# Kernel tuning notes

Measured on AMD Instinct MI355X. Metric: run time of the kernel, lower is better.

## Reference

```python
import jax, jax.numpy as jnp
import numpy as np

NUM_HEADS = 8
NG = 8  # group/grid size: seq = NG**3 = 512


def setup_inputs() -> dict:
    key = jax.random.key(0)
    k1, k2, k3 = jax.random.split(key, 3)
    batch, seq, chan = 32, NG ** 3, 512
    subspace_dim = 24
    x = jax.random.normal(k1, (batch, seq, chan), jnp.float32)
    # fixed symmetric-subspace basis (the free variable `conv_kernel` in the source)
    basis = jax.random.normal(k2, (seq, subspace_dim), jnp.float32)
    # learned param: (subspace_dim, num_heads), init stddev 0.01
    kernel = jax.random.normal(k3, (subspace_dim, NUM_HEADS), jnp.float32) * 0.01
    return {"x": x, "basis": basis, "kernel": kernel}


def reference(x, basis, kernel):
    batch, seq, chan = x.shape
    h, ng = NUM_HEADS, NG
    kn = 2 * ng - 1  # 15: circular tiling window
    ch = chan // h
    # 'batch (8 8 8) (ch h) -> h (batch ch) 8 8 8'
    x_im = x.reshape(batch, ng, ng, ng, ch, h)
    x_im = jnp.transpose(x_im, (5, 0, 4, 1, 2, 3)).reshape(h, batch * ch, ng, ng, ng)
    # circular tiling: tile 2x2x2 then crop to 2*ng-1 per axis; add trailing C=1
    x_im = jnp.tile(x_im, (1, 1, 2, 2, 2))[:, :, :kn, :kn, :kn, None]
    # expand subspace kernel: '(n n n) s, s h -> h n n n 1 1'
    kexp = jnp.einsum('gs,sh->hg', basis, kernel).reshape(h, ng, ng, ng, 1, 1)

    def conv(lhs, rhs):
        return jax.lax.conv_general_dilated(
            lhs, rhs, window_strides=(1, 1, 1), padding='VALID',
            dimension_numbers=('NXYZC', 'XYZIO', 'NXYZC'))

    # per-head VALID conv: [batch*ch, 15,15,15, 1] * [8,8,8,1,1] -> [batch*ch, 8,8,8, 1]
    out = jax.vmap(conv)(x_im, kexp)[..., 0]  # [h, batch*ch, 8, 8, 8]
    # 'h (batch ch) n n n -> batch (n n n) (ch h)'
    out = out.reshape(h, batch, ch, seq)
    out = jnp.transpose(out, (1, 3, 2, 0)).reshape(batch, seq, chan)
    return out
```

## Files before the change

### kernel.cpp

```cpp
#include <hip/hip_runtime.h>


#define S2C 0.70710678118654752f
#define SIGSTRIDE 577

template <bool INV>
__device__ __forceinline__ void dft8(float* R, float* I)
{
    float t0r = R[0] + R[4], t0i = I[0] + I[4];
    float t1r = R[1] + R[5], t1i = I[1] + I[5];
    float t2r = R[2] + R[6], t2i = I[2] + I[6];
    float t3r = R[3] + R[7], t3i = I[3] + I[7];
    float b0r = R[0] - R[4], b0i = I[0] - I[4];
    float d1r = R[1] - R[5], d1i = I[1] - I[5];
    float d2r = R[2] - R[6], d2i = I[2] - I[6];
    float d3r = R[3] - R[7], d3i = I[3] - I[7];
    float b1r, b1i, b2r, b2i, b3r, b3i;
    if (!INV) {
        b1r = (d1r + d1i) * S2C;  b1i = (d1i - d1r) * S2C;
        b2r = d2i;                b2i = -d2r;
        b3r = (d3i - d3r) * S2C;  b3i = -(d3r + d3i) * S2C;
    } else {
        b1r = (d1r - d1i) * S2C;  b1i = (d1i + d1r) * S2C;
        b2r = -d2i;               b2i = d2r;
        b3r = -(d3r + d3i) * S2C; b3i = (d3r - d3i) * S2C;
    }
    float u0r = t0r + t2r, u0i = t0i + t2i;
    float u1r = t1r + t3r, u1i = t1i + t3i;
    float u2r = t0r - t2r, u2i = t0i - t2i;
    float e3r = t1r - t3r, e3i = t1i - t3i;
    float u3r, u3i;
    if (!INV) { u3r = e3i;  u3i = -e3r; }
    else      { u3r = -e3i; u3i = e3r;  }
    R[0] = u0r + u1r; I[0] = u0i + u1i;
    R[4] = u0r - u1r; I[4] = u0i - u1i;
    R[2] = u2r + u3r; I[2] = u2i + u3i;
    R[6] = u2r - u3r; I[6] = u2i - u3i;
    float v0r = b0r + b2r, v0i = b0i + b2i;
    float v1r = b1r + b3r, v1i = b1i + b3i;
    float v2r = b0r - b2r, v2i = b0i - b2i;
    float w3r = b1r - b3r, w3i = b1i - b3i;
    float v3r, v3i;
    if (!INV) { v3r = w3i;  v3i = -w3r; }
    else      { v3r = -w3i; v3i = w3r;  }
    R[1] = v0r + v1r; I[1] = v0i + v1i;
    R[5] = v0r - v1r; I[5] = v0i - v1i;
    R[3] = v2r + v3r; I[3] = v2i + v3i;
    R[7] = v2r - v3r; I[7] = v2i - v3i;
}

__device__ const float CTAB8[8] = {1.f, S2C, 0.f, -S2C, -1.f, -S2C, 0.f, S2C};
__device__ const float STAB8[8] = {0.f, S2C, 1.f, S2C, 0.f, -S2C, -1.f, -S2C};

__global__ __launch_bounds__(256)
void eqfft_prep(const float* __restrict__ basis,
                const float* __restrict__ kparam,
                float2* __restrict__ V)
{
    __shared__ float Wl[512];
    __shared__ float CT[8], ST[8];
    const int tid = threadIdx.x;
    const int blk = blockIdx.x;
    const int h   = blk >> 4;
    if (tid < 8) { CT[tid] = CTAB8[tid]; ST[tid] = STAB8[tid]; }
    #pragma unroll
    for (int t = 0; t < 2; ++t) {
        const int g = tid * 2 + t;
        const float* bp = basis + g * 24;
        float acc = 0.f;
        #pragma unroll
        for (int s = 0; s < 24; ++s) acc += bp[s] * kparam[s * 8 + h];
        Wl[(g & 63) * 8 + (g >> 6)] = acc;
    }
    __syncthreads();
    const int f  = (blk & 15) * 32 + (tid >> 3);
    const int g1 = tid & 7;
    const int f1 = f >> 6, f2 = (f >> 3) & 7, f3 = f & 7;
    const int kb = (f1 * g1) & 7;
    float pr = 0.f, pi = 0.f;
    for (int g2 = 0; g2 < 8; ++g2) {
        const int k2 = kb + f2 * g2;
        const float* wrow = &Wl[g2 * 64 + g1];
        #pragma unroll
        for (int g3 = 0; g3 < 8; ++g3) {
            const int k = (k2 + f3 * g3) & 7;
            const float w = wrow[g3 * 8];
            pr += w * CT[k];
            pi += w * ST[k];
        }
    }
    pr += __shfl_xor(pr, 1); pi += __shfl_xor(pi, 1);
    pr += __shfl_xor(pr, 2); pi += __shfl_xor(pi, 2);
    pr += __shfl_xor(pr, 4); pi += __shfl_xor(pi, 4);
    if (g1 == 0)
        V[h * 512 + f] = make_float2(pr * (1.f / 512.f), pi * (1.f / 512.f));
}

__global__ __launch_bounds__(512, 6)
void eqfft_main(const float* __restrict__ x,
                const float2* __restrict__ V,
                float* __restrict__ out)
{
    __shared__ float reA[8 * SIGSTRIDE];
    __shared__ float imA[8 * SIGSTRIDE];

    const int tid  = threadIdx.x;
    const int bid  = blockIdx.x;
    const int L    = (bid & 7) * 256 + (bid >> 3);
    const int b    = L >> 6;
    const int ch0  = (L & 63) * 8;
    const int wid  = tid >> 6;
    const int lane = tid & 63;

    const float* xb = x  + (size_t)b * 262144 + ch0;
    float*       ob = out + (size_t)b * 262144 + ch0;

    #pragma unroll
    for (int i = 0; i < 2; ++i) {
        const int v  = i * 512 + tid;
        const int p  = v >> 1;
        const int c4 = (v & 1) * 4;
        const float4 d = *(const float4*)(xb + p * 512 + c4);
        const int base = (p >> 6) * 72 + ((p >> 3) & 7) * 9 + (p & 7);
        reA[(c4 + 0) * SIGSTRIDE + base] = d.x;
        reA[(c4 + 1) * SIGSTRIDE + base] = d.y;
        reA[(c4 + 2) * SIGSTRIDE + base] = d.z;
        reA[(c4 + 3) * SIGSTRIDE + base] = d.w;
    }
    __syncthreads();

    {
        const int base = wid * SIGSTRIDE + (lane >> 3) * 72 + (lane & 7) * 9;
        float R[8], I[8];
        #pragma unroll
        for (int j = 0; j < 8; ++j) { R[j] = reA[base + j]; I[j] = 0.f; }
        dft8<false>(R, I);
        #pragma unroll
        for (int j = 0; j < 8; ++j) { reA[base + j] = R[j]; imA[base + j] = I[j]; }
    }
    __syncthreads();

    {
        const int base = wid * SIGSTRIDE + (lane >> 3) * 72 + (lane & 7);
        float R[8], I[8];
        #pragma unroll
        for (int j = 0; j < 8; ++j) { R[j] = reA[base + j * 9]; I[j] = imA[base + j * 9]; }
        dft8<false>(R, I);
        #pragma unroll
        for (int j = 0; j < 8; ++j) { reA[base + j * 9] = R[j]; imA[base + j * 9] = I[j]; }
    }
    __syncthreads();

    {
        const int p2 = lane >> 3, p3 = lane & 7;
        const int base = wid * SIGSTRIDE + p2 * 9 + p3;
        const float2* vp = V + (wid << 9) + (p2 << 3) + p3;
        float R[8], I[8];
        #pragma unroll
        for (int j = 0; j < 8; ++j) { R[j] = reA[base + j * 72]; I[j] = imA[base + j * 72]; }
        dft8<false>(R, I);
        #pragma unroll
        for (int j = 0; j < 8; ++j) {
            const float2 v = vp[j << 6];
            const float nr = R[j] * v.x - I[j] * v.y;
            I[j] = R[j] * v.y + I[j] * v.x;
            R[j] = nr;
        }
        dft8<true>(R, I);
        #pragma unroll
        for (int j = 0; j < 8; ++j) { reA[base + j * 72] = R[j]; imA[base + j * 72] = I[j]; }
    }
    __syncthreads();

    {
        const int base = wid * SIGSTRIDE + (lane >> 3) * 72 + (lane & 7);
        float R[8], I[8];
        #pragma unroll
        for (int j = 0; j < 8; ++j) { R[j] = reA[base + j * 9]; I[j] = imA[base + j * 9]; }
        dft8<true>(R, I);
        #pragma unroll
        for (int j = 0; j < 8; ++j) { reA[base + j * 9] = R[j]; imA[base + j * 9] = I[j]; }
    }
    __syncthreads();

    {
        const int base = wid * SIGSTRIDE + (lane >> 3) * 72 + (lane & 7) * 9;
        float R[8], I[8];
        #pragma unroll
        for (int j = 0; j < 8; ++j) { R[j] = reA[base + j]; I[j] = imA[base + j]; }
        dft8<true>(R, I);
        #pragma unroll
        for (int j = 0; j < 8; ++j) { reA[base + j] = R[j]; }
    }
    __syncthreads();

    #pragma unroll
    for (int i = 0; i < 2; ++i) {
        const int v  = i * 512 + tid;
        const int p  = v >> 1;
        const int c4 = (v & 1) * 4;
        const int base = (p >> 6) * 72 + ((p >> 3) & 7) * 9 + (p & 7);
        float4 d;
        d.x = reA[(c4 + 0) * SIGSTRIDE + base];
        d.y = reA[(c4 + 1) * SIGSTRIDE + base];
        d.z = reA[(c4 + 2) * SIGSTRIDE + base];
        d.w = reA[(c4 + 3) * SIGSTRIDE + base];
        *(float4*)(ob + p * 512 + c4) = d;
    }
}

extern "C" void kernel_launch(void* const* d_in, const int* in_sizes, int n_in,
                              void* d_out, int out_size, void* d_ws, size_t ws_size,
                              hipStream_t stream)
{
    const float* x      = (const float*)d_in[0];
    const float* basis  = (const float*)d_in[1];
    const float* kparam = (const float*)d_in[2];
    float* out          = (float*)d_out;
    float2* V           = (float2*)d_ws;

    hipLaunchKernelGGL(eqfft_prep, dim3(128),  dim3(256), 0, stream, basis, kparam, V);
    hipLaunchKernelGGL(eqfft_main, dim3(2048), dim3(512), 0, stream, x, V, out);
}
```

Measured before the change: 98.13 us.

## Pack channel pairs interleaved in LDS and process two FFTs per thread

Reorganizes the shared-memory signal layout so each pair of channels is interleaved (float2), letting each thread run two 3D-FFT lines at once with vectorized float2/float4 LDS accesses. Block size drops from 512 to 256 threads with 3 blocks per CU, and the block-index swizzle is removed. This aims to cut LDS instruction count and bank traffic, and to raise per-thread ILP. The cost is more registers per thread and a different occupancy/L2 access pattern.

```diff
diff --git a/kernel.cpp b/kernel.cpp
--- a/kernel.cpp
+++ b/kernel.cpp
@@ -2,7 +2,9 @@
 
 
 #define S2C 0.70710678118654752f
-#define SIGSTRIDE 577
+#define ST2 20
+#define ST1 164
+#define STP 1312
 
 template <bool INV>
 __device__ __forceinline__ void dft8(float* R, float* I)
@@ -96,116 +98,155 @@
         V[h * 512 + f] = make_float2(pr * (1.f / 512.f), pi * (1.f / 512.f));
 }
 
-__global__ __launch_bounds__(512, 6)
+__global__ __launch_bounds__(256, 3)
 void eqfft_main(const float* __restrict__ x,
                 const float2* __restrict__ V,
                 float* __restrict__ out)
 {
-    __shared__ float reA[8 * SIGSTRIDE];
-    __shared__ float imA[8 * SIGSTRIDE];
-
-    const int tid  = threadIdx.x;
-    const int bid  = blockIdx.x;
-    const int L    = (bid & 7) * 256 + (bid >> 3);
-    const int b    = L >> 6;
-    const int ch0  = (L & 63) * 8;
-    const int wid  = tid >> 6;
-    const int lane = tid & 63;
-
-    const float* xb = x  + (size_t)b * 262144 + ch0;
+    __shared__ __align__(16) float reA[4 * STP];
+    __shared__ __align__(16) float imA[4 * STP];
+
+    const int tid = threadIdx.x;
+    const int bid = blockIdx.x;
+    const int b   = bid >> 6;
+    const int ch0 = (bid & 63) * 8;
+
+    const float* xb = x   + (size_t)b * 262144 + ch0;
     float*       ob = out + (size_t)b * 262144 + ch0;
 
     #pragma unroll
-    for (int i = 0; i < 2; ++i) {
-        const int v  = i * 512 + tid;
-        const int p  = v >> 1;
+    for (int i = 0; i < 4; ++i) {
+        const int v  = i * 256 + tid;
+        const int pt = v >> 1;
         const int c4 = (v & 1) * 4;
-        const float4 d = *(const float4*)(xb + p * 512 + c4);
-        const int base = (p >> 6) * 72 + ((p >> 3) & 7) * 9 + (p & 7);
-        reA[(c4 + 0) * SIGSTRIDE + base] = d.x;
-        reA[(c4 + 1) * SIGSTRIDE + base] = d.y;
-        reA[(c4 + 2) * SIGSTRIDE + base] = d.z;
-        reA[(c4 + 3) * SIGSTRIDE + base] = d.w;
-    }
-    __syncthreads();
-
-    {
-        const int base = wid * SIGSTRIDE + (lane >> 3) * 72 + (lane & 7) * 9;
-        float R[8], I[8];
-        #pragma unroll
-        for (int j = 0; j < 8; ++j) { R[j] = reA[base + j]; I[j] = 0.f; }
-        dft8<false>(R, I);
-        #pragma unroll
-        for (int j = 0; j < 8; ++j) { reA[base + j] = R[j]; imA[base + j] = I[j]; }
-    }
-    __syncthreads();
-
-    {
-        const int base = wid * SIGSTRIDE + (lane >> 3) * 72 + (lane & 7);
-        float R[8], I[8];
-        #pragma unroll
-        for (int j = 0; j < 8; ++j) { R[j] = reA[base + j * 9]; I[j] = imA[base + j * 9]; }
-        dft8<false>(R, I);
-        #pragma unroll
-        for (int j = 0; j < 8; ++j) { reA[base + j * 9] = R[j]; imA[base + j * 9] = I[j]; }
-    }
-    __syncthreads();
-
-    {
-        const int p2 = lane >> 3, p3 = lane & 7;
-        const int base = wid * SIGSTRIDE + p2 * 9 + p3;
-        const float2* vp = V + (wid << 9) + (p2 << 3) + p3;
-        float R[8], I[8];
-        #pragma unroll
-        for (int j = 0; j < 8; ++j) { R[j] = reA[base + j * 72]; I[j] = imA[base + j * 72]; }
-        dft8<false>(R, I);
-        #pragma unroll
-        for (int j = 0; j < 8; ++j) {
-            const float2 v = vp[j << 6];
-            const float nr = R[j] * v.x - I[j] * v.y;
-            I[j] = R[j] * v.y + I[j] * v.x;
-            R[j] = nr;
-        }
-        dft8<true>(R, I);
-        #pragma unroll
-        for (int j = 0; j < 8; ++j) { reA[base + j * 72] = R[j]; imA[base + j * 72] = I[j]; }
-    }
-    __syncthreads();
-
-    {
-        const int base = wid * SIGSTRIDE + (lane >> 3) * 72 + (lane & 7);
-        float R[8], I[8];
-        #pragma unroll
-        for (int j = 0; j < 8; ++j) { R[j] = reA[base + j * 9]; I[j] = imA[base + j * 9]; }
-        dft8<true>(R, I);
-        #pragma unroll
-        for (int j = 0; j < 8; ++j) { reA[base + j * 9] = R[j]; imA[base + j * 9] = I[j]; }
-    }
-    __syncthreads();
-
-    {
-        const int base = wid * SIGSTRIDE + (lane >> 3) * 72 + (lane & 7) * 9;
-        float R[8], I[8];
-        #pragma unroll
-        for (int j = 0; j < 8; ++j) { R[j] = reA[base + j]; I[j] = imA[base + j]; }
-        dft8<true>(R, I);
-        #pragma unroll
-        for (int j = 0; j < 8; ++j) { reA[base + j] = R[j]; }
+        const float4 d = *(const float4*)(xb + pt * 512 + c4);
+        const int base = (pt >> 6) * ST1 + ((pt >> 3) & 7) * ST2 + (pt & 7) * 2;
+        const int pr = c4 >> 1;
+        *(float2*)(reA + pr * STP + base)       = make_float2(d.x, d.y);
+        *(float2*)(reA + (pr + 1) * STP + base) = make_float2(d.z, d.w);
+    }
+    __syncthreads();
+
+    const int pair = tid >> 6;
+    const int line = tid & 63;
+    float R0[8], I0[8], R1[8], I1[8];
+
+    {
+        float* rp = reA + pair * STP + (line >> 3) * ST1 + (line & 7) * ST2;
+        float* ip = imA + pair * STP + (line >> 3) * ST1 + (line & 7) * ST2;
+        #pragma unroll
+        for (int k = 0; k < 4; ++k) {
+            const float4 d = *(const float4*)(rp + 4 * k);
+            R0[2*k] = d.x; R1[2*k] = d.y; R0[2*k+1] = d.z; R1[2*k+1] = d.w;
+            I0[2*k] = 0.f; I1[2*k] = 0.f; I0[2*k+1] = 0.f; I1[2*k+1] = 0.f;
+        }
+        dft8<false>(R0, I0); dft8<false>(R1, I1);
+        #pragma unroll
+        for (int k = 0; k < 4; ++k) {
+            *(float4*)(rp + 4*k) = make_float4(R0[2*k], R1[2*k], R0[2*k+1], R1[2*k+1]);
+            *(float4*)(ip + 4*k) = make_float4(I0[2*k], I1[2*k], I0[2*k+1], I1[2*k+1]);
+        }
+    }
+    __syncthreads();
+
+    {
+        float* rp = reA + pair * STP + (line >> 3) * ST1 + (line & 7) * 2;
+        float* ip = imA + pair * STP + (line >> 3) * ST1 + (line & 7) * 2;
+        #pragma unroll
+        for (int j = 0; j < 8; ++j) {
+            const float2 a = *(const float2*)(rp + j * ST2);
+            const float2 c = *(const float2*)(ip + j * ST2);
+            R0[j] = a.x; R1[j] = a.y; I0[j] = c.x; I1[j] = c.y;
+        }
+        dft8<false>(R0, I0); dft8<false>(R1, I1);
+        #pragma unroll
+        for (int j = 0; j < 8; ++j) {
+            *(float2*)(rp + j * ST2) = make_float2(R0[j], R1[j]);
+            *(float2*)(ip + j * ST2) = make_float2(I0[j], I1[j]);
+        }
+    }
+    __syncthreads();
+
+    {
+        const int p2 = line >> 3, p3 = line & 7;
+        const float2* v0 = V + (pair * 2 + 0) * 512 + p2 * 8 + p3;
+        const float2* v1 = V + (pair * 2 + 1) * 512 + p2 * 8 + p3;
+        float2 va[8], vb[8];
+        #pragma unroll
+        for (int j = 0; j < 8; ++j) { va[j] = v0[j << 6]; vb[j] = v1[j << 6]; }
+
+        float* rp = reA + pair * STP + p2 * ST2 + p3 * 2;
+        float* ip = imA + pair * STP + p2 * ST2 + p3 * 2;
+        #pragma unroll
+        for (int j = 0; j < 8; ++j) {
+            const float2 a = *(const float2*)(rp + j * ST1);
+            const float2 c = *(const float2*)(ip + j * ST1);
+            R0[j] = a.x; R1[j] = a.y; I0[j] = c.x; I1[j] = c.y;
+        }
+        dft8<false>(R0, I0); dft8<false>(R1, I1);
+        #pragma unroll
+        for (int j = 0; j < 8; ++j) {
+            float nr = R0[j] * va[j].x - I0[j] * va[j].y;
+            I0[j]    = R0[j] * va[j].y + I0[j] * va[j].x;
+            R0[j]    = nr;
+            nr       = R1[j] * vb[j].x - I1[j] * vb[j].y;
+            I1[j]    = R1[j] * vb[j].y + I1[j] * vb[j].x;
+            R1[j]    = nr;
+        }
+        dft8<true>(R0, I0); dft8<true>(R1, I1);
+        #pragma unroll
+        for (int j = 0; j < 8; ++j) {
+            *(float2*)(rp + j * ST1) = make_float2(R0[j], R1[j]);
+            *(float2*)(ip + j * ST1) = make_float2(I0[j], I1[j]);
+        }
+    }
+    __syncthreads();
+
+    {
+        float* rp = reA + pair * STP + (line >> 3) * ST1 + (line & 7) * 2;
+        float* ip = imA + pair * STP + (line >> 3) * ST1 + (line & 7) * 2;
+        #pragma unroll
+        for (int j = 0; j < 8; ++j) {
+            const float2 a = *(const float2*)(rp + j * ST2);
+            const float2 c = *(const float2*)(ip + j * ST2);
+            R0[j] = a.x; R1[j] = a.y; I0[j] = c.x; I1[j] = c.y;
+        }
+        dft8<true>(R0, I0); dft8<true>(R1, I1);
+        #pragma unroll
+        for (int j = 0; j < 8; ++j) {
+            *(float2*)(rp + j * ST2) = make_float2(R0[j], R1[j]);
+            *(float2*)(ip + j * ST2) = make_float2(I0[j], I1[j]);
+        }
+    }
+    __syncthreads();
+
+    {
+        float* rp = reA + pair * STP + (line >> 3) * ST1 + (line & 7) * ST2;
+        float* ip = imA + pair * STP + (line >> 3) * ST1 + (line & 7) * ST2;
+        #pragma unroll
+        for (int k = 0; k < 4; ++k) {
+            const float4 a = *(const float4*)(rp + 4 * k);
+            const float4 c = *(const float4*)(ip + 4 * k);
+            R0[2*k] = a.x; R1[2*k] = a.y; R0[2*k+1] = a.z; R1[2*k+1] = a.w;
+            I0[2*k] = c.x; I1[2*k] = c.y; I0[2*k+1] = c.z; I1[2*k+1] = c.w;
+        }
+        dft8<true>(R0, I0); dft8<true>(R1, I1);
+        #pragma unroll
+        for (int k = 0; k < 4; ++k)
+            *(float4*)(rp + 4*k) = make_float4(R0[2*k], R1[2*k], R0[2*k+1], R1[2*k+1]);
     }
     __syncthreads();
 
     #pragma unroll
-    for (int i = 0; i < 2; ++i) {
-        const int v  = i * 512 + tid;
-        const int p  = v >> 1;
+    for (int i = 0; i < 4; ++i) {
+        const int v  = i * 256 + tid;
+        const int pt = v >> 1;
         const int c4 = (v & 1) * 4;
-        const int base = (p >> 6) * 72 + ((p >> 3) & 7) * 9 + (p & 7);
-        float4 d;
-        d.x = reA[(c4 + 0) * SIGSTRIDE + base];
-        d.y = reA[(c4 + 1) * SIGSTRIDE + base];
-        d.z = reA[(c4 + 2) * SIGSTRIDE + base];
-        d.w = reA[(c4 + 3) * SIGSTRIDE + base];
-        *(float4*)(ob + p * 512 + c4) = d;
+        const int base = (pt >> 6) * ST1 + ((pt >> 3) & 7) * ST2 + (pt & 7) * 2;
+        const int pr = c4 >> 1;
+        const float2 a = *(const float2*)(reA + pr * STP + base);
+        const float2 c = *(const float2*)(reA + (pr + 1) * STP + base);
+        *(float4*)(ob + pt * 512 + c4) = make_float4(a.x, a.y, c.x, c.y);
     }
 }
 
@@ -220,5 +261,5 @@
     float2* V           = (float2*)d_ws;
 
     hipLaunchKernelGGL(eqfft_prep, dim3(128),  dim3(256), 0, stream, basis, kparam, V);
-    hipLaunchKernelGGL(eqfft_main, dim3(2048), dim3(512), 0, stream, x, V, out);
-}
+    hipLaunchKernelGGL(eqfft_main, dim3(2048), dim3(256), 0, stream, x, V, out);
+}
```

Result: slower. 113.8 us (+16.0%).

## Pack two real channels per complex FFT and interleave re/im in LDS

Applied to the files above, without the earlier changes.

Instead of running a complex 3D FFT on each real channel with zero imaginary part, the kernel packs two channels that share a head (c and c+8) into the real and imaginary parts of one complex signal. This halves the FFT work and the thread count per block. Re/im are interleaved in LDS so reads and writes can use float2/float4. Block-to-tile mapping and channel grouping are redone so each block handles four heads with paired channels. This relies on the filter being real so the two outputs can be separated from the real and imaginary parts, and the new LDS strides may change bank conflicts.

```diff
diff --git a/kernel.cpp b/kernel.cpp
--- a/kernel.cpp
+++ b/kernel.cpp
@@ -1,8 +1,10 @@
 #include <hip/hip_runtime.h>
 
 
-#define S2C 0.70710678118654752f
-#define SIGSTRIDE 577
+#define S2C  0.70710678118654752f
+#define LS2  16
+#define LS1  132
+#define LCST 1056
 
 template <bool INV>
 __device__ __forceinline__ void dft8(float* R, float* I)
@@ -96,116 +98,123 @@
         V[h * 512 + f] = make_float2(pr * (1.f / 512.f), pi * (1.f / 512.f));
 }
 
-__global__ __launch_bounds__(512, 6)
+__global__ __launch_bounds__(256, 6)
 void eqfft_main(const float* __restrict__ x,
                 const float2* __restrict__ V,
                 float* __restrict__ out)
 {
-    __shared__ float reA[8 * SIGSTRIDE];
-    __shared__ float imA[8 * SIGSTRIDE];
-
-    const int tid  = threadIdx.x;
-    const int bid  = blockIdx.x;
-    const int L    = (bid & 7) * 256 + (bid >> 3);
-    const int b    = L >> 6;
-    const int ch0  = (L & 63) * 8;
-    const int wid  = tid >> 6;
-    const int lane = tid & 63;
-
-    const float* xb = x  + (size_t)b * 262144 + ch0;
-    float*       ob = out + (size_t)b * 262144 + ch0;
+    __shared__ __align__(16) float lds[4 * LCST];
+
+    const int tid = threadIdx.x;
+    const int d   = blockIdx.x;
+    const int T   = (d & 7) * 2 + ((d >> 3) & 1) + (d >> 4) * 16;
+    const int b   = T >> 6;
+    const int r   = T & 63;
+    const int c0  = (r >> 1) * 16 + (r & 1) * 4;
+
+    const float* xb = x   + (size_t)b * 262144 + c0;
+    float*       ob = out + (size_t)b * 262144 + c0;
 
     #pragma unroll
     for (int i = 0; i < 2; ++i) {
-        const int v  = i * 512 + tid;
-        const int p  = v >> 1;
-        const int c4 = (v & 1) * 4;
-        const float4 d = *(const float4*)(xb + p * 512 + c4);
-        const int base = (p >> 6) * 72 + ((p >> 3) & 7) * 9 + (p & 7);
-        reA[(c4 + 0) * SIGSTRIDE + base] = d.x;
-        reA[(c4 + 1) * SIGSTRIDE + base] = d.y;
-        reA[(c4 + 2) * SIGSTRIDE + base] = d.z;
-        reA[(c4 + 3) * SIGSTRIDE + base] = d.w;
-    }
-    __syncthreads();
-
-    {
-        const int base = wid * SIGSTRIDE + (lane >> 3) * 72 + (lane & 7) * 9;
-        float R[8], I[8];
-        #pragma unroll
-        for (int j = 0; j < 8; ++j) { R[j] = reA[base + j]; I[j] = 0.f; }
+        const int p = i * 256 + tid;
+        const float4 A  = *(const float4*)(xb + p * 512);
+        const float4 Bv = *(const float4*)(xb + p * 512 + 8);
+        float* dst = lds + (p >> 6) * LS1 + ((p >> 3) & 7) * LS2 + (p & 7) * 2;
+        *(float2*)(dst + 0 * LCST) = make_float2(A.x, Bv.x);
+        *(float2*)(dst + 1 * LCST) = make_float2(A.y, Bv.y);
+        *(float2*)(dst + 2 * LCST) = make_float2(A.z, Bv.z);
+        *(float2*)(dst + 3 * LCST) = make_float2(A.w, Bv.w);
+    }
+    __syncthreads();
+
+    const int q    = tid >> 6;
+    const int lane = tid & 63;
+    const int hi   = lane >> 3, lo = lane & 7;
+    float* const cb = lds + q * LCST;
+    float R[8], I[8];
+
+    {
+        float* pp = cb + hi * LS1 + lo * LS2;
+        #pragma unroll
+        for (int k = 0; k < 4; ++k) {
+            const float4 z = *(const float4*)(pp + 4 * k);
+            R[2*k] = z.x; I[2*k] = z.y; R[2*k+1] = z.z; I[2*k+1] = z.w;
+        }
         dft8<false>(R, I);
         #pragma unroll
-        for (int j = 0; j < 8; ++j) { reA[base + j] = R[j]; imA[base + j] = I[j]; }
-    }
-    __syncthreads();
-
-    {
-        const int base = wid * SIGSTRIDE + (lane >> 3) * 72 + (lane & 7);
-        float R[8], I[8];
-        #pragma unroll
-        for (int j = 0; j < 8; ++j) { R[j] = reA[base + j * 9]; I[j] = imA[base + j * 9]; }
+        for (int k = 0; k < 4; ++k)
+            *(float4*)(pp + 4 * k) = make_float4(R[2*k], I[2*k], R[2*k+1], I[2*k+1]);
+    }
+    __syncthreads();
+
+    {
+        float* pp = cb + hi * LS1 + lo * 2;
+        #pragma unroll
+        for (int j = 0; j < 8; ++j) { const float2 z = *(const float2*)(pp + j * LS2); R[j] = z.x; I[j] = z.y; }
         dft8<false>(R, I);
         #pragma unroll
-        for (int j = 0; j < 8; ++j) { reA[base + j * 9] = R[j]; imA[base + j * 9] = I[j]; }
-    }
-    __syncthreads();
-
-    {
-        const int p2 = lane >> 3, p3 = lane & 7;
-        const int base = wid * SIGSTRIDE + p2 * 9 + p3;
-        const float2* vp = V + (wid << 9) + (p2 << 3) + p3;
-        float R[8], I[8];
-        #pragma unroll
-        for (int j = 0; j < 8; ++j) { R[j] = reA[base + j * 72]; I[j] = imA[base + j * 72]; }
+        for (int j = 0; j < 8; ++j) *(float2*)(pp + j * LS2) = make_float2(R[j], I[j]);
+    }
+    __syncthreads();
+
+    {
+        const int h = ((r & 1) << 2) + q;
+        const float2* vp = V + h * 512 + lane;
+        float2 va[8];
+        #pragma unroll
+        for (int j = 0; j < 8; ++j) va[j] = vp[j * 64];
+
+        float* pp = cb + hi * LS2 + lo * 2;
+        #pragma unroll
+        for (int j = 0; j < 8; ++j) { const float2 z = *(const float2*)(pp + j * LS1); R[j] = z.x; I[j] = z.y; }
         dft8<false>(R, I);
         #pragma unroll
         for (int j = 0; j < 8; ++j) {
-            const float2 v = vp[j << 6];
-            const float nr = R[j] * v.x - I[j] * v.y;
-            I[j] = R[j] * v.y + I[j] * v.x;
+            const float nr = R[j] * va[j].x - I[j] * va[j].y;
+            I[j] = R[j] * va[j].y + I[j] * va[j].x;
             R[j] = nr;
         }
         dft8<true>(R, I);
         #pragma unroll
-        for (int j = 0; j < 8; ++j) { reA[base + j * 72] = R[j]; imA[base + j * 72] = I[j]; }
-    }
-    __syncthreads();
-
-    {
-        const int base = wid * SIGSTRIDE + (lane >> 3) * 72 + (lane & 7);
-        float R[8], I[8];
-        #pragma unroll
-        for (int j = 0; j < 8; ++j) { R[j] = reA[base + j * 9]; I[j] = imA[base + j * 9]; }
+        for (int j = 0; j < 8; ++j) *(float2*)(pp + j * LS1) = make_float2(R[j], I[j]);
+    }
+    __syncthreads();
+
+    {
+        float* pp = cb + hi * LS1 + lo * 2;
+        #pragma unroll
+        for (int j = 0; j < 8; ++j) { const float2 z = *(const float2*)(pp + j * LS2); R[j] = z.x; I[j] = z.y; }
         dft8<true>(R, I);
         #pragma unroll
-        for (int j = 0; j < 8; ++j) { reA[base + j * 9] = R[j]; imA[base + j * 9] = I[j]; }
-    }
-    __syncthreads();
-
-    {
-        const int base = wid * SIGSTRIDE + (lane >> 3) * 72 + (lane & 7) * 9;
-        float R[8], I[8];
-        #pragma unroll
-        for (int j = 0; j < 8; ++j) { R[j] = reA[base + j]; I[j] = imA[base + j]; }
+        for (int j = 0; j < 8; ++j) *(float2*)(pp + j * LS2) = make_float2(R[j], I[j]);
+    }
+    __syncthreads();
+
+    {
+        float* pp = cb + hi * LS1 + lo * LS2;
+        #pragma unroll
+        for (int k = 0; k < 4; ++k) {
+            const float4 z = *(const float4*)(pp + 4 * k);
+            R[2*k] = z.x; I[2*k] = z.y; R[2*k+1] = z.z; I[2*k+1] = z.w;
+        }
         dft8<true>(R, I);
         #pragma unroll
-        for (int j = 0; j < 8; ++j) { reA[base + j] = R[j]; }
+        for (int k = 0; k < 4; ++k)
+            *(float4*)(pp + 4 * k) = make_float4(R[2*k], I[2*k], R[2*k+1], I[2*k+1]);
     }
     __syncthreads();
 
     #pragma unroll
     for (int i = 0; i < 2; ++i) {
-        const int v  = i * 512 + tid;
-        const int p  = v >> 1;
-        const int c4 = (v & 1) * 4;
-        const int base = (p >> 6) * 72 + ((p >> 3) & 7) * 9 + (p & 7);
-        float4 d;
-        d.x = reA[(c4 + 0) * SIGSTRIDE + base];
-        d.y = reA[(c4 + 1) * SIGSTRIDE + base];
-        d.z = reA[(c4 + 2) * SIGSTRIDE + base];
-        d.w = reA[(c4 + 3) * SIGSTRIDE + base];
-        *(float4*)(ob + p * 512 + c4) = d;
+        const int p = i * 256 + tid;
+        const float* src = lds + (p >> 6) * LS1 + ((p >> 3) & 7) * LS2 + (p & 7) * 2;
+        const float2 z0 = *(const float2*)(src + 0 * LCST);
+        const float2 z1 = *(const float2*)(src + 1 * LCST);
+        const float2 z2 = *(const float2*)(src + 2 * LCST);
+        const float2 z3 = *(const float2*)(src + 3 * LCST);
+        *(float4*)(ob + p * 512)     = make_float4(z0.x, z1.x, z2.x, z3.x);
+        *(float4*)(ob + p * 512 + 8) = make_float4(z0.y, z1.y, z2.y, z3.y);
     }
 }
 
@@ -220,5 +229,5 @@
     float2* V           = (float2*)d_ws;
 
     hipLaunchKernelGGL(eqfft_prep, dim3(128),  dim3(256), 0, stream, basis, kparam, V);
-    hipLaunchKernelGGL(eqfft_main, dim3(2048), dim3(512), 0, stream, x, V, out);
-}
+    hipLaunchKernelGGL(eqfft_main, dim3(2048), dim3(256), 0, stream, x, V, out);
+}
```

Result: slower. 102.2 us (+4.1%).
